# Optimization experiments

Measured on AMD Instinct MI355X. Metric: run time of the kernel, lower is better.

Reference implementation:

```python
import jax, jax.numpy as jnp
import numpy as np

S, B, D = 2048, 2, 2048
H, C = 16, 128  # heads, dim_head
EPS = 1e-6


def _rmsnorm(x, w):
    # per-head RMSNorm, computed in float32 like the torch module
    xf = x.astype(jnp.float32)
    var = jnp.mean(xf * xf, axis=-1, keepdims=True)
    return (xf * jax.lax.rsqrt(var + EPS) * w).astype(x.dtype)


def _rope(x, freqs):
    # x: [S,B,H,C], freqs: [S,C] raw frequencies
    cos = jnp.cos(freqs)[:, None, None, :].astype(x.dtype)
    sin = jnp.sin(freqs)[:, None, None, :].astype(x.dtype)
    x1, x2 = jnp.split(x, 2, axis=-1)
    rot = jnp.concatenate((-x2, x1), axis=-1)
    return x * cos + rot * sin


def setup_inputs() -> dict:
    key = jax.random.key(0)
    ks = jax.random.split(key, 6)
    scale = 0.02
    return {
        "x": jax.random.normal(ks[0], (S, B, D), jnp.float32),
        "rope_emb": jax.random.normal(ks[1], (S, 1, 1, C), jnp.float32),
        "Wq": jax.random.normal(ks[2], (D, D), jnp.float32) * scale,
        "Wk": jax.random.normal(ks[3], (D, D), jnp.float32) * scale,
        "Wv": jax.random.normal(ks[4], (D, D), jnp.float32) * scale,
        "Wout": jax.random.normal(ks[5], (D, D), jnp.float32) * scale,
        "q_scale": jnp.ones((C,), jnp.float32),
        "k_scale": jnp.ones((C,), jnp.float32),
    }


def reference(x, rope_emb, Wq, Wk, Wv, Wout, q_scale, k_scale):
    s, b, _ = x.shape
    freqs = rope_emb.reshape(s, C)  # squeeze(1).squeeze(1)

    # QKV projections (no bias), split heads: [S,B,H,C]
    q = (x @ Wq.T).reshape(s, b, H, C)
    k = (x @ Wk.T).reshape(s, b, H, C)
    v = (x @ Wv.T).reshape(s, b, H, C)

    # per-head RMSNorm on q, k; identity on v (qkv_norm='RRI')
    q = _rmsnorm(q, q_scale)
    k = _rmsnorm(k, k_scale)

    # RoPE on q, k (self-attention)
    q = _rope(q, freqs)
    k = _rope(k, freqs)

    # SDPA, non-causal
    inv_scale = 1.0 / jnp.sqrt(jnp.asarray(C, x.dtype))
    scores = jnp.einsum('sbnc,tbnc->bnst', q, k) * inv_scale  # [B,H,S,S]
    probs = jax.nn.softmax(scores, axis=-1)
    out = jnp.einsum('bnst,tbnc->sbnc', probs, v)  # [S,B,H,C]

    # output projection (no bias, dropout inactive)
    return out.reshape(s, b, H * C) @ Wout.T
```

## Files before the change

### kernel.cpp

```cpp
#include <hip/hip_runtime.h>
#include <stdint.h>

#define S_DIM 2048
#define B_DIM 2
#define D_DIM 2048
#define H_DIM 16
#define C_DIM 128
#define M_DIM 4096

typedef __bf16 bf16x8 __attribute__((ext_vector_type(8)));
typedef float f32x4 __attribute__((ext_vector_type(4)));
typedef unsigned short u16x4 __attribute__((ext_vector_type(4)));
typedef unsigned short u16x8 __attribute__((ext_vector_type(8)));

__device__ __forceinline__ float bf2f(unsigned short u) {
    union { unsigned int i; float f; } c; c.i = ((unsigned int)u) << 16; return c.f;
}
__device__ __forceinline__ unsigned short f2bf(float f) {
    union { float f; unsigned int i; } c; c.f = f;
    unsigned int r = c.i + 0x7FFFu + ((c.i >> 16) & 1u);
    return (unsigned short)(r >> 16);
}

__global__ void rope_tables_k(const float* __restrict__ freqs,
                              float* __restrict__ ctab, float* __restrict__ stab, int n) {
    int i = blockIdx.x * blockDim.x + threadIdx.x;
    if (i < n) { float f = freqs[i]; ctab[i] = cosf(f); stab[i] = sinf(f); }
}

__global__ void cast_all_k(const float* __restrict__ x,
                           const float* __restrict__ w0, const float* __restrict__ w1,
                           const float* __restrict__ w2, const float* __restrict__ w3,
                           unsigned short* __restrict__ xb, unsigned short* __restrict__ wb) {
    const int nx4 = (M_DIM * D_DIM) / 4;
    const int nw4 = (D_DIM * D_DIM) / 4;
    const int total = nx4 + 4 * nw4;
    int stride = gridDim.x * blockDim.x;
    for (int i = blockIdx.x * blockDim.x + threadIdx.x; i < total; i += stride) {
        const float* src; unsigned short* dst; int idx;
        if (i < nx4) { src = x; dst = xb; idx = i; }
        else {
            int j = i - nx4;
            int sel = j >> 20;
            idx = j & (nw4 - 1);
            src = (sel == 0) ? w0 : (sel == 1) ? w1 : (sel == 2) ? w2 : w3;
            dst = wb + (size_t)sel * (size_t)D_DIM * D_DIM;
        }
        float4 v = reinterpret_cast<const float4*>(src)[idx];
        ushort4 o;
        o.x = f2bf(v.x); o.y = f2bf(v.y); o.z = f2bf(v.z); o.w = f2bf(v.w);
        reinterpret_cast<ushort4*>(dst)[idx] = o;
    }
}

template <typename OutT, int BN>
__global__ __launch_bounds__(512) void gemm8_k(
    const unsigned short* __restrict__ A,
    const unsigned short* __restrict__ Bm,
    OutT* __restrict__ C,
    int M, int N, int K)
{
    constexpr int NFR = BN / 64;
    constexpr int WNS = BN / 4;
    constexpr int BCH = BN / 64 * 512;
    __shared__ __align__(16) unsigned short ldsA[2][256 * 64];
    __shared__ __align__(16) unsigned short ldsB[2][BN * 64];

    const int tid  = threadIdx.x;
    const int wave = tid >> 6;
    const int lane = tid & 63;
    const int wm = wave >> 2;
    const int wn = wave & 3;
    const int g  = lane >> 4;
    const int ro = lane & 15;

    const int nwg = gridDim.x * gridDim.y;
    int lin = blockIdx.y * gridDim.x + blockIdx.x;
    lin = (lin & 7) * (nwg >> 3) + (lin >> 3);
    const int brow = (lin % gridDim.x) * 256;
    const int bcol = (lin / gridDim.x) * BN;
    const int NT = K >> 6;

    const unsigned short* As = A  + (size_t)brow * K;
    const unsigned short* Bs = Bm + (size_t)bcol * K;

    f32x4 acc[8][NFR] = {};

    auto stageA = [&](int T) {
        const int buf = T & 1;
        #pragma unroll
        for (int j = 0; j < 4; ++j) {
            const int slot = j * 512 + tid;
            const int row = slot >> 3, c = slot & 7;
            __builtin_amdgcn_global_load_lds(
                (const __attribute__((address_space(1))) void*)(
                    As + (size_t)row * K + T * 64 + ((c ^ (row & 7)) << 3)),
                (__attribute__((address_space(3))) void*)(
                    &ldsA[buf][(j * 512 + wave * 64) * 8]),
                16, 0, 0);
        }
    };
    auto stageB = [&](int T) {
        const int buf = T & 1;
        #pragma unroll
        for (int j = 0; j < BCH / 512; ++j) {
            const int slot = j * 512 + tid;
            const int row = slot >> 3, c = slot & 7;
            __builtin_amdgcn_global_load_lds(
                (const __attribute__((address_space(1))) void*)(
                    Bs + (size_t)row * K + T * 64 + ((c ^ (row & 7)) << 3)),
                (__attribute__((address_space(3))) void*)(
                    &ldsB[buf][(j * 512 + wave * 64) * 8]),
                16, 0, 0);
        }
    };

    auto rdA = [&](int buf, int mi, int ks) -> bf16x8 {
        const int row = wm * 128 + mi * 16 + ro;
        return *reinterpret_cast<const bf16x8*>(
            &ldsA[buf][row * 64 + (((ks * 4 + g) ^ (row & 7)) << 3)]);
    };
    auto rdB = [&](int buf, int ni, int ks) -> bf16x8 {
        const int row = wn * WNS + ni * 16 + ro;
        return *reinterpret_cast<const bf16x8*>(
            &ldsB[buf][row * 64 + (((ks * 4 + g) ^ (row & 7)) << 3)]);
    };

    stageB(0);
    stageA(0);
    stageB(1);
    asm volatile("s_waitcnt vmcnt(6)" ::: "memory");
    __builtin_amdgcn_s_barrier();

    for (int T = 0; T < NT; ++T) {
        const int buf = T & 1;
        bf16x8 bfr[NFR];

        #pragma unroll
        for (int i = 0; i < NFR; ++i) bfr[i] = rdB(buf, i, 0);
        if (T + 1 < NT) stageA(T + 1);
        __builtin_amdgcn_s_barrier();
        __builtin_amdgcn_s_setprio(1);
        #pragma unroll
        for (int mi = 0; mi < 4; ++mi) {
            bf16x8 af = rdA(buf, mi, 0);
            #pragma unroll
            for (int ni = 0; ni < NFR; ++ni)
                acc[mi][ni] = __builtin_amdgcn_mfma_f32_16x16x32_bf16(af, bfr[ni], acc[mi][ni], 0, 0, 0);
        }
        __builtin_amdgcn_s_setprio(0);
        __builtin_amdgcn_s_barrier();

        __builtin_amdgcn_s_setprio(1);
        #pragma unroll
        for (int mi = 0; mi < 4; ++mi) {
            bf16x8 af = rdA(buf, 4 + mi, 0);
            #pragma unroll
            for (int ni = 0; ni < NFR; ++ni)
                acc[4 + mi][ni] = __builtin_amdgcn_mfma_f32_16x16x32_bf16(af, bfr[ni], acc[4 + mi][ni], 0, 0, 0);
        }
        __builtin_amdgcn_s_setprio(0);
        __builtin_amdgcn_s_barrier();

        #pragma unroll
        for (int i = 0; i < NFR; ++i) bfr[i] = rdB(buf, i, 1);
        __builtin_amdgcn_s_barrier();
        __builtin_amdgcn_s_setprio(1);
        #pragma unroll
        for (int mi = 0; mi < 4; ++mi) {
            bf16x8 af = rdA(buf, mi, 1);
            #pragma unroll
            for (int ni = 0; ni < NFR; ++ni)
                acc[mi][ni] = __builtin_amdgcn_mfma_f32_16x16x32_bf16(af, bfr[ni], acc[mi][ni], 0, 0, 0);
        }
        __builtin_amdgcn_s_setprio(0);
        __builtin_amdgcn_s_barrier();

        if (T + 2 < NT) stageB(T + 2);
        if (T + 1 < NT) {
            if (T + 2 < NT) asm volatile("s_waitcnt vmcnt(6)" ::: "memory");
            else            asm volatile("s_waitcnt vmcnt(0)" ::: "memory");
        }
        __builtin_amdgcn_s_setprio(1);
        #pragma unroll
        for (int mi = 0; mi < 4; ++mi) {
            bf16x8 af = rdA(buf, 4 + mi, 1);
            #pragma unroll
            for (int ni = 0; ni < NFR; ++ni)
                acc[4 + mi][ni] = __builtin_amdgcn_mfma_f32_16x16x32_bf16(af, bfr[ni], acc[4 + mi][ni], 0, 0, 0);
        }
        __builtin_amdgcn_s_setprio(0);
        __builtin_amdgcn_s_barrier();
    }

    const int rg = g * 4;
    #pragma unroll
    for (int mi = 0; mi < 8; ++mi) {
        #pragma unroll
        for (int r = 0; r < 4; ++r) {
            const int row = brow + wm * 128 + mi * 16 + rg + r;
            const size_t base = (size_t)row * N + bcol + wn * WNS;
            #pragma unroll
            for (int ni = 0; ni < NFR; ++ni) {
                float v = acc[mi][ni][r];
                if constexpr (sizeof(OutT) == 2) C[base + ni * 16 + ro] = f2bf(v);
                else                             C[base + ni * 16 + ro] = v;
            }
        }
    }
}

template <typename OutT>
__global__ __launch_bounds__(512) void gemm_v4_k(
    const unsigned short* __restrict__ A,
    const unsigned short* __restrict__ Bm,
    OutT* __restrict__ C,
    int M, int N, int K)
{
    constexpr int ATILE = 128 * 64;
    constexpr int BTILE = 256 * 64;
    __shared__ __align__(16) unsigned short ldsA[3 * ATILE];
    __shared__ __align__(16) unsigned short ldsB[3 * BTILE];

    const int tid  = threadIdx.x;
    const int wave = tid >> 6;
    const int lane = tid & 63;
    const int wm = wave >> 2;
    const int wn = wave & 3;
    const int g  = lane >> 4;
    const int ro = lane & 15;

    const int nwg = gridDim.x * gridDim.y;
    int lin = blockIdx.y * gridDim.x + blockIdx.x;
    lin = (lin & 7) * (nwg >> 3) + (lin >> 3);
    const int brow = (lin % gridDim.x) * 128;
    const int bcol = (lin / gridDim.x) * 256;
    const int NT = K >> 6;

    const unsigned short* As = A  + (size_t)brow * K;
    const unsigned short* Bs = Bm + (size_t)bcol * K;

    f32x4 acc[4][4] = {};

    auto stage = [&](int buf, int t) {
        #pragma unroll
        for (int j = 0; j < 2; ++j) {
            const int slot = j * 512 + tid;
            const int row = slot >> 3, c = slot & 7;
            __builtin_amdgcn_global_load_lds(
                (const __attribute__((address_space(1))) void*)(
                    As + (size_t)row * K + t * 64 + ((c ^ (row & 7)) << 3)),
                (__attribute__((address_space(3))) void*)(
                    ldsA + buf * ATILE + (j * 512 + wave * 64) * 8),
                16, 0, 0);
        }
        #pragma unroll
        for (int j = 0; j < 4; ++j) {
            const int slot = j * 512 + tid;
            const int row = slot >> 3, c = slot & 7;
            __builtin_amdgcn_global_load_lds(
                (const __attribute__((address_space(1))) void*)(
                    Bs + (size_t)row * K + t * 64 + ((c ^ (row & 7)) << 3)),
                (__attribute__((address_space(3))) void*)(
                    ldsB + buf * BTILE + (j * 512 + wave * 64) * 8),
                16, 0, 0);
        }
    };

    auto rdA = [&](int buf, int mi, int ks) -> bf16x8 {
        const int row = wm * 64 + mi * 16 + ro;
        const int c = (ks * 4 + g) ^ (row & 7);
        return *reinterpret_cast<const bf16x8*>(ldsA + buf * ATILE + row * 64 + c * 8);
    };
    auto rdB = [&](int buf, int ni, int ks) -> bf16x8 {
        const int row = wn * 64 + ni * 16 + ro;
        const int c = (ks * 4 + g) ^ (row & 7);
        return *reinterpret_cast<const bf16x8*>(ldsB + buf * BTILE + row * 64 + c * 8);
    };

    stage(0, 0);
    stage(1, 1);
    asm volatile("s_waitcnt vmcnt(6)" ::: "memory");
    __builtin_amdgcn_s_barrier();

    int cb = 0;
    for (int t = 0; t < NT; ++t) {
        #pragma unroll
        for (int ks = 0; ks < 2; ++ks) {
            bf16x8 af[4], bf[4];
            #pragma unroll
            for (int i = 0; i < 4; ++i) af[i] = rdA(cb, i, ks);
            #pragma unroll
            for (int i = 0; i < 4; ++i) bf[i] = rdB(cb, i, ks);
            if (ks == 0) {
                if (t + 2 < NT) stage((cb == 0) ? 2 : cb - 1, t + 2);
            } else {
                if (t + 2 < NT) asm volatile("s_waitcnt vmcnt(6)" ::: "memory");
                else            asm volatile("s_waitcnt vmcnt(0)" ::: "memory");
            }
            __builtin_amdgcn_s_barrier();
            asm volatile("s_waitcnt lgkmcnt(0)" ::: "memory");
            __builtin_amdgcn_sched_barrier(0);
            __builtin_amdgcn_s_setprio(1);
            #pragma unroll
            for (int mi = 0; mi < 4; ++mi)
                #pragma unroll
                for (int ni = 0; ni < 4; ++ni)
                    acc[mi][ni] = __builtin_amdgcn_mfma_f32_16x16x32_bf16(
                        af[mi], bf[ni], acc[mi][ni], 0, 0, 0);
            __builtin_amdgcn_s_setprio(0);
            __builtin_amdgcn_s_barrier();
        }
        cb = (cb == 2) ? 0 : cb + 1;
    }

    const int rg = g * 4;
    #pragma unroll
    for (int mi = 0; mi < 4; ++mi) {
        #pragma unroll
        for (int r = 0; r < 4; ++r) {
            const int row = brow + wm * 64 + mi * 16 + rg + r;
            const size_t base = (size_t)row * N + bcol + wn * 64;
            #pragma unroll
            for (int ni = 0; ni < 4; ++ni) {
                float v = acc[mi][ni][r];
                if constexpr (sizeof(OutT) == 2) C[base + ni * 16 + ro] = f2bf(v);
                else                             C[base + ni * 16 + ro] = v;
            }
        }
    }
}

__global__ __launch_bounds__(256) void qk_post2_k(
    const unsigned short* __restrict__ rawQKV, int ld,
    const float* __restrict__ q_scale, const float* __restrict__ k_scale,
    const float* __restrict__ ctab, const float* __restrict__ stab,
    unsigned short* __restrict__ Qb, unsigned short* __restrict__ Kb,
    float inv_scale)
{
    const int isK = blockIdx.y;
    const unsigned short* raw = rawQKV + (isK ? D_DIM : 0);
    const float* wscale = isK ? k_scale : q_scale;
    unsigned short* outp = isK ? Kb : Qb;
    const float post_mul = isK ? 1.0f : inv_scale;

    const int gw = blockIdx.x * 4 + (threadIdx.x >> 6);
    const int lane = threadIdx.x & 63;
    const int m = gw >> 4;
    const int h = gw & 15;
    const int s = m >> 1, b = m & 1;
    const int c0 = lane * 2;

    const unsigned short* src = raw + (size_t)m * ld + h * C_DIM + c0;
    unsigned int packed = *reinterpret_cast<const unsigned int*>(src);
    float x0 = bf2f((unsigned short)(packed & 0xFFFF));
    float x1 = bf2f((unsigned short)(packed >> 16));

    float ss = x0 * x0 + x1 * x1;
    #pragma unroll
    for (int off = 32; off; off >>= 1) ss += __shfl_xor(ss, off);
    const float rs = rsqrtf(ss * (1.0f / C_DIM) + 1e-6f);

    float n0 = x0 * rs * wscale[c0];
    float n1 = x1 * rs * wscale[c0 + 1];
    float p0 = __shfl_xor(n0, 32);
    float p1 = __shfl_xor(n1, 32);
    const float sgn = (lane < 32) ? -1.0f : 1.0f;
    const float* cp = ctab + (size_t)s * C_DIM + c0;
    const float* sp = stab + (size_t)s * C_DIM + c0;
    float o0 = (n0 * cp[0] + sgn * p0 * sp[0]) * post_mul;
    float o1 = (n1 * cp[1] + sgn * p1 * sp[1]) * post_mul;

    unsigned int opk = (unsigned int)f2bf(o0) | ((unsigned int)f2bf(o1) << 16);
    *reinterpret_cast<unsigned int*>(
        outp + ((size_t)(b * H_DIM + h) * S_DIM + s) * C_DIM + c0) = opk;
}

__global__ __launch_bounds__(256) void v_transpose_k(
    const unsigned short* __restrict__ raw, int ld, int colbase,
    unsigned short* __restrict__ Vt)
{
    __shared__ __align__(16) unsigned short tile[64][136];
    const int bh = blockIdx.y;
    const int b = bh >> 4, h = bh & 15;
    const int sbase = blockIdx.x * 64;
    const int t = threadIdx.x;

    {
        const int s = t >> 2, cq = (t & 3) * 32;
        const unsigned short* src = raw + (size_t)((sbase + s) * B_DIM + b) * ld + colbase + h * C_DIM + cq;
        #pragma unroll
        for (int j = 0; j < 4; ++j) {
            u16x8 v = *reinterpret_cast<const u16x8*>(src + j * 8);
            *reinterpret_cast<u16x8*>(&tile[s][cq + j * 8]) = v;
        }
    }
    __syncthreads();
    {
        const int c = t >> 1, sh = (t & 1) * 32;
        unsigned short* dst = Vt + ((size_t)bh * C_DIM + c) * S_DIM + sbase + sh;
        #pragma unroll
        for (int j = 0; j < 32; j += 8) {
            u16x8 o;
            #pragma unroll
            for (int e = 0; e < 8; ++e) o[e] = tile[sh + j + e][c];
            *reinterpret_cast<u16x8*>(dst + j) = o;
        }
    }
}

__global__ __launch_bounds__(512, 2) void attn_k(
    const unsigned short* __restrict__ Qb,
    const unsigned short* __restrict__ Kb,
    const unsigned short* __restrict__ Vt,
    unsigned short* __restrict__ Ao)
{
    __shared__ __align__(16) unsigned short ldsK[2][64 * 128];
    __shared__ __align__(16) unsigned short ldsV[2][128 * 64];
    __shared__ __align__(16) unsigned short plds[8][32 * 64];

    const int bh = blockIdx.y;
    const int wave = threadIdx.x >> 6;
    const int lane = threadIdx.x & 63;
    const int qbase = blockIdx.x * 256 + wave * 32;
    const int g  = lane >> 4;
    const int ro = lane & 15;
    const int ko = g * 8;
    const int rg = g * 4;

    const unsigned short* Q  = Qb + (size_t)bh * S_DIM * C_DIM;
    const unsigned short* Km = Kb + (size_t)bh * S_DIM * C_DIM;
    const unsigned short* V  = Vt + (size_t)bh * C_DIM * S_DIM;
    unsigned short* pw = &plds[wave][0];

    bf16x8 qf[2][4];
    #pragma unroll
    for (int mq = 0; mq < 2; ++mq)
        #pragma unroll
        for (int kf = 0; kf < 4; ++kf)
            qf[mq][kf] = *reinterpret_cast<const bf16x8*>(
                Q + (size_t)(qbase + mq * 16 + ro) * C_DIM + kf * 32 + ko);

    bf16x8 ones;
    #pragma unroll
    for (int e = 0; e < 8; ++e) ones[e] = (__bf16)1.0f;

    auto stage = [&](int bufi, int kb) {
        #pragma unroll
        for (int j = 0; j < 2; ++j) {
            const int idx = (wave * 2 + j) * 64 + lane;
            {
                const int row = idx >> 4, ch = idx & 15;
                const int sch = (ch & 8) | ((ch ^ row) & 7);
                __builtin_amdgcn_global_load_lds(
                    (const __attribute__((address_space(1))) void*)(
                        Km + (size_t)(kb + row) * C_DIM + sch * 8),
                    (__attribute__((address_space(3))) void*)(
                        &ldsK[bufi][(wave * 2 + j) * 512]),
                    16, 0, 0);
            }
            {
                const int row = idx >> 3, ch = idx & 7;
                const int sch = (ch ^ row) & 7;
                __builtin_amdgcn_global_load_lds(
                    (const __attribute__((address_space(1))) void*)(
                        V + (size_t)row * S_DIM + kb + sch * 8),
                    (__attribute__((address_space(3))) void*)(
                        &ldsV[bufi][(wave * 2 + j) * 512]),
                    16, 0, 0);
            }
        }
    };

    f32x4 of[2][8] = {};
    f32x4 osum[2] = {};
    float mrow[2] = {-1e30f, -1e30f};

    stage(0, 0);
    asm volatile("s_waitcnt vmcnt(0)" ::: "memory");
    __syncthreads();

    int cur = 0;
    for (int kb = 0; kb < S_DIM; kb += 64) {
        if (kb + 64 < S_DIM) stage(cur ^ 1, kb + 64);

        f32x4 s4[2][4] = {};
        __builtin_amdgcn_s_setprio(1);
        #pragma unroll
        for (int nc = 0; nc < 4; ++nc) {
            const int r_loc = nc * 16 + ro;
            bf16x8 kfr[4];
            #pragma unroll
            for (int kf = 0; kf < 4; ++kf) {
                const int c = kf * 4 + g;
                const int sch = (c & 8) | ((c ^ r_loc) & 7);
                kfr[kf] = *reinterpret_cast<const bf16x8*>(&ldsK[cur][r_loc * 128 + sch * 8]);
            }
            #pragma unroll
            for (int mq = 0; mq < 2; ++mq)
                #pragma unroll
                for (int kf = 0; kf < 4; ++kf)
                    s4[mq][nc] = __builtin_amdgcn_mfma_f32_16x16x32_bf16(
                        kfr[kf], qf[mq][kf], s4[mq][nc], 0, 0, 0);
        }
        __builtin_amdgcn_s_setprio(0);

        float mx[2];
        #pragma unroll
        for (int mq = 0; mq < 2; ++mq) {
            float m0 = fmaxf(fmaxf(s4[mq][0][0], s4[mq][0][1]), fmaxf(s4[mq][0][2], s4[mq][0][3]));
            #pragma unroll
            for (int nc = 1; nc < 4; ++nc) {
                float mn = fmaxf(fmaxf(s4[mq][nc][0], s4[mq][nc][1]),
                                 fmaxf(s4[mq][nc][2], s4[mq][nc][3]));
                m0 = fmaxf(m0, mn);
            }
            m0 = fmaxf(m0, __shfl_xor(m0, 16));
            m0 = fmaxf(m0, __shfl_xor(m0, 32));
            mx[mq] = m0;
        }

        if (__any(fmaxf(mx[0] - mrow[0], mx[1] - mrow[1]) > 8.0f)) {
            #pragma unroll
            for (int mq = 0; mq < 2; ++mq) {
                float mnew = fmaxf(mrow[mq], mx[mq]);
                float dm = mrow[mq] - mnew;
                mrow[mq] = mnew;
                #pragma unroll
                for (int r = 0; r < 4; ++r) {
                    float dr = __shfl(dm, (lane & 48) | (rg + r));
                    float rs = __expf(dr);
                    osum[mq][r] *= rs;
                    #pragma unroll
                    for (int nf = 0; nf < 8; ++nf) of[mq][nf][r] *= rs;
                }
            }
        }

        #pragma unroll
        for (int mq = 0; mq < 2; ++mq) {
            const int qrow = mq * 16 + ro;
            #pragma unroll
            for (int nc = 0; nc < 4; ++nc) {
                u16x4 pk;
                #pragma unroll
                for (int r = 0; r < 4; ++r)
                    pk[r] = f2bf(__expf(s4[mq][nc][r] - mrow[mq]));
                const int chunk = 2 * nc + (g >> 1);
                *reinterpret_cast<u16x4*>(
                    &pw[qrow * 64 + ((chunk ^ (ro & 7)) << 3) + 4 * (g & 1)]) = pk;
            }
        }
        __asm__ volatile("" ::: "memory");

        __builtin_amdgcn_s_setprio(1);
        #pragma unroll
        for (int ks = 0; ks < 2; ++ks) {
            bf16x8 pa[2];
            #pragma unroll
            for (int mq = 0; mq < 2; ++mq) {
                const int qrow = mq * 16 + ro;
                pa[mq] = *reinterpret_cast<const bf16x8*>(
                    &pw[qrow * 64 + (((ks * 4 + g) ^ (ro & 7)) << 3)]);
            }
            #pragma unroll
            for (int nf = 0; nf < 8; ++nf) {
                const int vr = nf * 16 + ro;
                const int sch = (ks * 4 + g) ^ (vr & 7);
                bf16x8 vf = *reinterpret_cast<const bf16x8*>(&ldsV[cur][vr * 64 + sch * 8]);
                #pragma unroll
                for (int mq = 0; mq < 2; ++mq)
                    of[mq][nf] = __builtin_amdgcn_mfma_f32_16x16x32_bf16(pa[mq], vf, of[mq][nf], 0, 0, 0);
            }
            #pragma unroll
            for (int mq = 0; mq < 2; ++mq)
                osum[mq] = __builtin_amdgcn_mfma_f32_16x16x32_bf16(pa[mq], ones, osum[mq], 0, 0, 0);
        }
        __builtin_amdgcn_s_setprio(0);

        asm volatile("s_waitcnt vmcnt(0)" ::: "memory");
        __syncthreads();
        cur ^= 1;
    }

    const int b = bh >> 4, h = bh & 15;
    #pragma unroll
    for (int mq = 0; mq < 2; ++mq) {
        #pragma unroll
        for (int r = 0; r < 4; ++r) {
            const float inv_l = 1.0f / osum[mq][r];
            const int srow = qbase + mq * 16 + rg + r;
            unsigned short* dst = Ao + (size_t)(srow * B_DIM + b) * D_DIM + h * C_DIM;
            #pragma unroll
            for (int nf = 0; nf < 8; ++nf)
                dst[nf * 16 + ro] = f2bf(of[mq][nf][r] * inv_l);
        }
    }
}

extern "C" void kernel_launch(void* const* d_in, const int* in_sizes, int n_in,
                              void* d_out, int out_size, void* d_ws, size_t ws_size,
                              hipStream_t stream) {
    const float* x       = (const float*)d_in[0];
    const float* rope    = (const float*)d_in[1];
    const float* Wq      = (const float*)d_in[2];
    const float* Wk      = (const float*)d_in[3];
    const float* Wv      = (const float*)d_in[4];
    const float* Wo      = (const float*)d_in[5];
    const float* q_scale = (const float*)d_in[6];
    const float* k_scale = (const float*)d_in[7];
    float* out = (float*)d_out;

    char* w = (char*)d_ws;
    size_t off = 0;
    auto alloc = [&](size_t bytes) {
        char* p = w + off; off += (bytes + 255) & ~(size_t)255; return p;
    };
    unsigned short* xb   = (unsigned short*)alloc((size_t)M_DIM * D_DIM * 2);
    unsigned short* Wqb  = (unsigned short*)alloc((size_t)4 * D_DIM * D_DIM * 2);
    unsigned short* Wob  = Wqb + (size_t)3 * D_DIM * D_DIM;
    unsigned short* rawQKV = (unsigned short*)alloc((size_t)M_DIM * 3 * D_DIM * 2);
    unsigned short* Qb   = (unsigned short*)alloc((size_t)M_DIM * D_DIM * 2);
    unsigned short* Kb   = (unsigned short*)alloc((size_t)M_DIM * D_DIM * 2);
    unsigned short* Vt   = (unsigned short*)alloc((size_t)M_DIM * D_DIM * 2);
    float* ctab = (float*)alloc((size_t)S_DIM * C_DIM * 4);
    float* stab = (float*)alloc((size_t)S_DIM * C_DIM * 4);
    unsigned short* Ao = rawQKV;
    (void)ws_size; (void)in_sizes; (void)n_in; (void)out_size;

    const int NQKV = 3 * D_DIM;
    const float inv_scale = 0.08838834764831845f;

    rope_tables_k<<<(S_DIM * C_DIM + 255) / 256, 256, 0, stream>>>(rope, ctab, stab, S_DIM * C_DIM);
    cast_all_k<<<2048, 256, 0, stream>>>(x, Wq, Wk, Wv, Wo, xb, Wqb);

    gemm8_k<unsigned short, 384><<<dim3(M_DIM / 256, NQKV / 384), 512, 0, stream>>>(
        xb, Wqb, rawQKV, M_DIM, NQKV, D_DIM);

    qk_post2_k<<<dim3(M_DIM * H_DIM / 4, 2), 256, 0, stream>>>(
        rawQKV, NQKV, q_scale, k_scale, ctab, stab, Qb, Kb, inv_scale);
    v_transpose_k<<<dim3(S_DIM / 64, B_DIM * H_DIM), 256, 0, stream>>>(rawQKV, NQKV, 2 * D_DIM, Vt);

    attn_k<<<dim3(S_DIM / 256, B_DIM * H_DIM), 512, 0, stream>>>(Qb, Kb, Vt, Ao);

    gemm_v4_k<float><<<dim3(M_DIM / 128, D_DIM / 256), 512, 0, stream>>>(
        Ao, Wob, out, M_DIM, D_DIM, D_DIM);
}
```

Before: 295.7 us.

## Prefetch A fragments before MFMA bursts and halve attention block size

In the QKV GEMM, all A-fragment LDS reads for each quarter-step are now issued ahead of time, followed by an lgkmcnt(0) wait and a sched_barrier, so the MFMA burst runs without interleaved LDS latency. An extra block barrier is added before each burst. Separately, the attention kernel goes from 512 to 256 threads per block, with 128 queries per block and each wave staging twice as many K/V chunks. This doubles the grid, which should give better CU occupancy and balance, at the cost of loading K/V twice as often per query.

```diff
diff --git a/kernel.cpp b/kernel.cpp
--- a/kernel.cpp
+++ b/kernel.cpp
@@ -134,61 +134,71 @@
 
     for (int T = 0; T < NT; ++T) {
         const int buf = T & 1;
-        bf16x8 bfr[NFR];
+        bf16x8 bfr[NFR], af[4];
 
         #pragma unroll
         for (int i = 0; i < NFR; ++i) bfr[i] = rdB(buf, i, 0);
+        #pragma unroll
+        for (int i = 0; i < 4; ++i) af[i] = rdA(buf, i, 0);
         if (T + 1 < NT) stageA(T + 1);
         __builtin_amdgcn_s_barrier();
+        asm volatile("s_waitcnt lgkmcnt(0)" ::: "memory");
+        __builtin_amdgcn_sched_barrier(0);
         __builtin_amdgcn_s_setprio(1);
         #pragma unroll
-        for (int mi = 0; mi < 4; ++mi) {
-            bf16x8 af = rdA(buf, mi, 0);
+        for (int mi = 0; mi < 4; ++mi)
             #pragma unroll
             for (int ni = 0; ni < NFR; ++ni)
-                acc[mi][ni] = __builtin_amdgcn_mfma_f32_16x16x32_bf16(af, bfr[ni], acc[mi][ni], 0, 0, 0);
-        }
+                acc[mi][ni] = __builtin_amdgcn_mfma_f32_16x16x32_bf16(af[mi], bfr[ni], acc[mi][ni], 0, 0, 0);
         __builtin_amdgcn_s_setprio(0);
         __builtin_amdgcn_s_barrier();
 
+        #pragma unroll
+        for (int i = 0; i < 4; ++i) af[i] = rdA(buf, 4 + i, 0);
+        __builtin_amdgcn_s_barrier();
+        asm volatile("s_waitcnt lgkmcnt(0)" ::: "memory");
+        __builtin_amdgcn_sched_barrier(0);
         __builtin_amdgcn_s_setprio(1);
         #pragma unroll
-        for (int mi = 0; mi < 4; ++mi) {
-            bf16x8 af = rdA(buf, 4 + mi, 0);
+        for (int mi = 0; mi < 4; ++mi)
             #pragma unroll
             for (int ni = 0; ni < NFR; ++ni)
-                acc[4 + mi][ni] = __builtin_amdgcn_mfma_f32_16x16x32_bf16(af, bfr[ni], acc[4 + mi][ni], 0, 0, 0);
-        }
+                acc[4 + mi][ni] = __builtin_amdgcn_mfma_f32_16x16x32_bf16(af[mi], bfr[ni], acc[4 + mi][ni], 0, 0, 0);
         __builtin_amdgcn_s_setprio(0);
         __builtin_amdgcn_s_barrier();
 
         #pragma unroll
         for (int i = 0; i < NFR; ++i) bfr[i] = rdB(buf, i, 1);
-        __builtin_amdgcn_s_barrier();
+        #pragma unroll
+        for (int i = 0; i < 4; ++i) af[i] = rdA(buf, i, 1);
+        __builtin_amdgcn_s_barrier();
+        asm volatile("s_waitcnt lgkmcnt(0)" ::: "memory");
+        __builtin_amdgcn_sched_barrier(0);
         __builtin_amdgcn_s_setprio(1);
         #pragma unroll
-        for (int mi = 0; mi < 4; ++mi) {
-            bf16x8 af = rdA(buf, mi, 1);
+        for (int mi = 0; mi < 4; ++mi)
             #pragma unroll
             for (int ni = 0; ni < NFR; ++ni)
-                acc[mi][ni] = __builtin_amdgcn_mfma_f32_16x16x32_bf16(af, bfr[ni], acc[mi][ni], 0, 0, 0);
-        }
+                acc[mi][ni] = __builtin_amdgcn_mfma_f32_16x16x32_bf16(af[mi], bfr[ni], acc[mi][ni], 0, 0, 0);
         __builtin_amdgcn_s_setprio(0);
         __builtin_amdgcn_s_barrier();
 
+        #pragma unroll
+        for (int i = 0; i < 4; ++i) af[i] = rdA(buf, 4 + i, 1);
         if (T + 2 < NT) stageB(T + 2);
         if (T + 1 < NT) {
             if (T + 2 < NT) asm volatile("s_waitcnt vmcnt(6)" ::: "memory");
             else            asm volatile("s_waitcnt vmcnt(0)" ::: "memory");
         }
+        __builtin_amdgcn_s_barrier();
+        asm volatile("s_waitcnt lgkmcnt(0)" ::: "memory");
+        __builtin_amdgcn_sched_barrier(0);
         __builtin_amdgcn_s_setprio(1);
         #pragma unroll
-        for (int mi = 0; mi < 4; ++mi) {
-            bf16x8 af = rdA(buf, 4 + mi, 1);
+        for (int mi = 0; mi < 4; ++mi)
             #pragma unroll
             for (int ni = 0; ni < NFR; ++ni)
-                acc[4 + mi][ni] = __builtin_amdgcn_mfma_f32_16x16x32_bf16(af, bfr[ni], acc[4 + mi][ni], 0, 0, 0);
-        }
+                acc[4 + mi][ni] = __builtin_amdgcn_mfma_f32_16x16x32_bf16(af[mi], bfr[ni], acc[4 + mi][ni], 0, 0, 0);
         __builtin_amdgcn_s_setprio(0);
         __builtin_amdgcn_s_barrier();
     }
@@ -409,7 +419,7 @@
     }
 }
 
-__global__ __launch_bounds__(512, 2) void attn_k(
+__global__ __launch_bounds__(256, 2) void attn_k(
     const unsigned short* __restrict__ Qb,
     const unsigned short* __restrict__ Kb,
     const unsigned short* __restrict__ Vt,
@@ -417,12 +427,12 @@
 {
     __shared__ __align__(16) unsigned short ldsK[2][64 * 128];
     __shared__ __align__(16) unsigned short ldsV[2][128 * 64];
-    __shared__ __align__(16) unsigned short plds[8][32 * 64];
+    __shared__ __align__(16) unsigned short plds[4][32 * 64];
 
     const int bh = blockIdx.y;
     const int wave = threadIdx.x >> 6;
     const int lane = threadIdx.x & 63;
-    const int qbase = blockIdx.x * 256 + wave * 32;
+    const int qbase = blockIdx.x * 128 + wave * 32;
     const int g  = lane >> 4;
     const int ro = lane & 15;
     const int ko = g * 8;
@@ -447,8 +457,8 @@
 
     auto stage = [&](int bufi, int kb) {
         #pragma unroll
-        for (int j = 0; j < 2; ++j) {
-            const int idx = (wave * 2 + j) * 64 + lane;
+        for (int j = 0; j < 4; ++j) {
+            const int idx = (wave * 4 + j) * 64 + lane;
             {
                 const int row = idx >> 4, ch = idx & 15;
                 const int sch = (ch & 8) | ((ch ^ row) & 7);
@@ -456,7 +466,7 @@
                     (const __attribute__((address_space(1))) void*)(
                         Km + (size_t)(kb + row) * C_DIM + sch * 8),
                     (__attribute__((address_space(3))) void*)(
-                        &ldsK[bufi][(wave * 2 + j) * 512]),
+                        &ldsK[bufi][(wave * 4 + j) * 512]),
                     16, 0, 0);
             }
             {
@@ -466,7 +476,7 @@
                     (const __attribute__((address_space(1))) void*)(
                         V + (size_t)row * S_DIM + kb + sch * 8),
                     (__attribute__((address_space(3))) void*)(
-                        &ldsV[bufi][(wave * 2 + j) * 512]),
+                        &ldsV[bufi][(wave * 4 + j) * 512]),
                     16, 0, 0);
             }
         }
@@ -641,7 +651,7 @@
         rawQKV, NQKV, q_scale, k_scale, ctab, stab, Qb, Kb, inv_scale);
     v_transpose_k<<<dim3(S_DIM / 64, B_DIM * H_DIM), 256, 0, stream>>>(rawQKV, NQKV, 2 * D_DIM, Vt);
 
-    attn_k<<<dim3(S_DIM / 256, B_DIM * H_DIM), 512, 0, stream>>>(Qb, Kb, Vt, Ao);
+    attn_k<<<dim3(S_DIM / 128, B_DIM * H_DIM), 256, 0, stream>>>(Qb, Kb, Vt, Ao);
 
     gemm_v4_k<float><<<dim3(M_DIM / 128, D_DIM / 256), 512, 0, stream>>>(
         Ao, Wob, out, M_DIM, D_DIM, D_DIM);
```

Result: slower. 303.2 us (+2.6%).
